# Optimization experiments

Hardware: AMD Instinct MI355X
Metric: run time of the kernel (lower is better)

The kernel has to match this reference:

```python
import jax, jax.numpy as jnp
import numpy as np

EMB = 256
HEADS = 4
HD = EMB // HEADS
BS, SZ = 4, 64


def _layernorm(x, g, b, eps=1e-5):
    mu = jnp.mean(x, axis=-1, keepdims=True)
    var = jnp.mean((x - mu) ** 2, axis=-1, keepdims=True)
    return (x - mu) * jax.lax.rsqrt(var + eps) * g + b


def setup_inputs() -> dict:
    key = jax.random.key(0)
    ks = jax.random.split(key, 12)
    s = lambda k, shape, sc: jax.random.normal(k, shape, jnp.float32) * sc
    return {
        "x": s(ks[0], (BS, EMB, SZ, SZ), 1.0),
        "ln1_g": jnp.ones((EMB,), jnp.float32),
        "ln1_b": jnp.zeros((EMB,), jnp.float32),
        "wq": s(ks[1], (HD, HD), HD ** -0.5), "bq": jnp.zeros((HD,), jnp.float32),
        "wk": s(ks[2], (HD, HD), HD ** -0.5), "bk": jnp.zeros((HD,), jnp.float32),
        "wv": s(ks[3], (HD, HD), HD ** -0.5), "bv": jnp.zeros((HD,), jnp.float32),
        "wo": s(ks[4], (EMB, EMB), EMB ** -0.5), "bo": jnp.zeros((EMB,), jnp.float32),
        "ln2_g": jnp.ones((EMB,), jnp.float32),
        "ln2_b": jnp.zeros((EMB,), jnp.float32),
        "w1": s(ks[5], (EMB, EMB), EMB ** -0.5), "b1": jnp.zeros((EMB,), jnp.float32),
        "w2": s(ks[6], (EMB, EMB), EMB ** -0.5), "b2": jnp.zeros((EMB,), jnp.float32),
    }


def reference(x, ln1_g, ln1_b, wq, bq, wk, bk, wv, bv, wo, bo, ln2_g, ln2_b, w1, b1, w2, b2):
    bs, c, sz, _ = x.shape
    seq = sz * sz
    xt = x.reshape(bs, c, seq).swapaxes(1, 2)  # [b, s, c]
    xn = _layernorm(xt, ln1_g, ln1_b)
    # split heads: [b, h, s, d]
    h = xn.reshape(bs, seq, HEADS, HD).transpose(0, 2, 1, 3)
    q = h @ wq + bq
    k = h @ wk + bk
    v = h @ wv + bv
    scores = jnp.einsum("bhqd,bhkd->bhqk", q, k) / (HD ** 0.5)
    attn = jax.nn.softmax(scores, axis=-1)
    o = jnp.einsum("bhqk,bhkd->bhqd", attn, v)
    o = o.transpose(0, 2, 1, 3).reshape(bs, seq, c)
    o = o @ wo + bo
    av = o + xt  # residual 1
    ff = _layernorm(av, ln2_g, ln2_b) @ w1 + b1
    ff = jax.nn.gelu(ff, approximate=False) @ w2 + b2
    out = ff + av  # residual 2
    return out.swapaxes(1, 2).reshape(bs, c, sz, sz)
```

## Files before the change

### kernel.cpp

```cpp
#include <hip/hip_runtime.h>
#include <hip/hip_bf16.h>
#include <cstdint>

typedef __attribute__((ext_vector_type(8))) short short8;
typedef __attribute__((ext_vector_type(4))) short short4_;
typedef __attribute__((ext_vector_type(4))) float float4_;

#define MFMA16(a,b,c)  __builtin_amdgcn_mfma_f32_16x16x32_bf16(a,b,c,0,0,0)
#define MFMA16K16(a,b,c) __builtin_amdgcn_mfma_f32_16x16x16bf16_1k(a,b,c,0,0,0)
#define EXP2(x) __builtin_amdgcn_exp2f(x)

__device__ __forceinline__ short f2bs(float f) {
    union { float f; uint32_t u; } c;
    c.f = f;
    c.u += 0x7FFF + ((c.u >> 16) & 1);
    return (short)(c.u >> 16);
}
__device__ __forceinline__ float s2f(short s) {
    union { uint32_t u; float f; } c;
    c.u = ((uint32_t)(uint16_t)s) << 16;
    return c.f;
}

static const int EMB = 256;
static const int SEQ = 4096;
static const int TOK = 16384;

#define QSCALE 0.18033688011112042f

__global__ __launch_bounds__(256) void repack_kernel(
    const float* wq, const float* wk, const float* wv,
    const float* wo, const float* w1, const float* w2,
    short* wqT, short* wkT, short* wvT, short* woT, short* w1T, short* w2T)
{
    int idx = blockIdx.x * 256 + threadIdx.x;
    if (idx < 3 * 4096) {
        int m = idx / 4096, r = idx % 4096;
        int n = r / 64, k = r % 64;
        const float* src = (m == 0) ? wq : (m == 1) ? wk : wv;
        short* dst = (m == 0) ? wqT : (m == 1) ? wkT : wvT;
        float v = src[k * 64 + n];
        if (m == 0) v *= QSCALE;
        dst[n * 64 + k] = f2bs(v);
    } else {
        int idx2 = idx - 3 * 4096;
        if (idx2 < 3 * 65536) {
            int m = idx2 / 65536, r = idx2 % 65536;
            int n = r / 256, k = r % 256;
            const float* src = (m == 0) ? wo : (m == 1) ? w1 : w2;
            short* dst = (m == 0) ? woT : (m == 1) ? w1T : w2T;
            dst[n * 256 + k] = f2bs(src[k * 256 + n]);
        }
    }
}

__global__ __launch_bounds__(64) void ln1_kernel(
    const float* x, const float* g, const float* bta,
    short* xn, short* xt)
{
    int t = blockIdx.x * 64 + threadIdx.x;
    int b = t >> 12, sp = t & 4095;
    const float* xb = x + (size_t)b * EMB * SEQ + sp;
    float sum = 0.f, ss = 0.f;
#pragma unroll 32
    for (int c = 0; c < 256; c++) {
        float v = xb[(size_t)c * SEQ];
        sum += v; ss += v * v;
    }
    float mu = sum * (1.f / 256.f);
    float var = ss * (1.f / 256.f) - mu * mu;
    float rs = rsqrtf(var + 1e-5f);
    short* xnr = xn + (size_t)t * 256;
    short* xtr = xt + (size_t)t * 256;
#pragma unroll 8
    for (int c = 0; c < 256; c += 4) {
        short4_ ra, na;
#pragma unroll
        for (int j = 0; j < 4; j++) {
            float v = xb[(size_t)(c + j) * SEQ];
            ra[j] = f2bs(v);
            na[j] = f2bs((v - mu) * rs * g[c + j] + bta[c + j]);
        }
        *(short4_*)(xtr + c) = ra;
        *(short4_*)(xnr + c) = na;
    }
}

__global__ __launch_bounds__(256) void qkv_kernel(
    const short* xn, const short* wqT, const short* wkT, const short* wvT,
    const float* bq, const float* bk, const float* bv,
    short* qo, short* ko, short* vto)
{
    int tid = threadIdx.x;
    int w = tid >> 6, lane = tid & 63, quad = lane >> 4, l15 = lane & 15;
    int m0 = blockIdx.x * 64 + w * 16;
    int row = m0 + l15;
    int bb = row >> 12;
    int s0 = (m0 & 4095) + quad * 4;

    short8 a0[4], a1[4];
#pragma unroll
    for (int h = 0; h < 4; h++) {
        a0[h] = *(const short8*)(xn + (size_t)row * 256 + h * 64 + quad * 8);
        a1[h] = *(const short8*)(xn + (size_t)row * 256 + h * 64 + 32 + quad * 8);
    }

#pragma unroll
    for (int p = 0; p < 3; p++) {
        const short* WT = (p == 0) ? wqT : (p == 1) ? wkT : wvT;
        const float* bias = (p == 0) ? bq : (p == 1) ? bk : bv;
        float bscale = (p == 0) ? QSCALE : 1.f;
#pragma unroll
        for (int nb = 0; nb < 4; nb++) {
            int col = nb * 16 + l15;
            short8 b0 = *(const short8*)(WT + col * 64 + quad * 8);
            short8 b1 = *(const short8*)(WT + col * 64 + 32 + quad * 8);
            float bvv = bias[col] * bscale;
#pragma unroll
            for (int h = 0; h < 4; h++) {
                float4_ acc = {bvv, bvv, bvv, bvv};
                acc = MFMA16(a0[h], b0, acc);
                acc = MFMA16(a1[h], b1, acc);
                size_t headbase = (size_t)(bb * 4 + h) * SEQ;
                if (p < 2) {
                    short* dst = (p == 0) ? qo : ko;
#pragma unroll
                    for (int r = 0; r < 4; r++)
                        dst[(headbase + s0 + r) * 64 + col] = f2bs(acc[r]);
                } else {
                    short4_ pk;
#pragma unroll
                    for (int r = 0; r < 4; r++) pk[r] = f2bs(acc[r]);
                    *(short4_*)(vto + ((size_t)(bb * 4 + h) * 64 + col) * SEQ + s0) = pk;
                }
            }
        }
    }
}

__global__ __attribute__((amdgpu_flat_work_group_size(256, 256),
                          amdgpu_waves_per_eu(4, 4)))
void flash_kernel(
    const short* q, const short* k, const short* vt,
    short* O0, short* O1, float* l0, float* l1)
{
    __shared__ short K_lds[64 * 64];
    __shared__ short V_lds[64 * 64];

    int tid = threadIdx.x;
    int w = tid >> 6, lane = tid & 63, quad = lane >> 4, l15 = lane & 15;
    int qt = blockIdx.x, bh = blockIdx.y, grp = blockIdx.z;
    int span = 64 / gridDim.z;

    const short* qb = q + (size_t)bh * SEQ * 64;
    const short* kb = k + (size_t)bh * SEQ * 64 + (size_t)grp * span * 64 * 64;
    const short* vb = vt + (size_t)bh * 64 * SEQ + grp * span * 64;

    int qrow0 = qt * 128 + w * 32 + l15;
    int qrow1 = qrow0 + 16;
    short8 qA0 = *(const short8*)(qb + (size_t)qrow0 * 64 + quad * 8);
    short8 qA1 = *(const short8*)(qb + (size_t)qrow0 * 64 + 32 + quad * 8);
    short8 qB0 = *(const short8*)(qb + (size_t)qrow1 * 64 + quad * 8);
    short8 qB1 = *(const short8*)(qb + (size_t)qrow1 * 64 + 32 + quad * 8);

    float4_ oacc0[4], oacc1[4];
#pragma unroll
    for (int md = 0; md < 4; md++) {
        oacc0[md] = {0.f, 0.f, 0.f, 0.f};
        oacc1[md] = {0.f, 0.f, 0.f, 0.f};
    }
    float li0 = 0.f, li1 = 0.f;

    int srow = tid >> 2;
    int sr7 = srow & 7;
    int c0 = tid & 3;
    int l7 = l15 & 7;

    int dcA = (c0 ^ sr7) << 3;
    int dcB = ((c0 + 4) ^ sr7) << 3;

    short8 kr0 = *(const short8*)(kb + (size_t)srow * 64 + c0 * 8);
    short8 kr1 = *(const short8*)(kb + (size_t)srow * 64 + (c0 + 4) * 8);
    short8 vr0 = *(const short8*)(vb + (size_t)srow * SEQ + c0 * 8);
    short8 vr1 = *(const short8*)(vb + (size_t)srow * SEQ + (c0 + 4) * 8);

    for (int kt = 0; kt < span; kt++) {
        __syncthreads();
        *(short8*)&K_lds[srow * 64 + dcA] = kr0;
        *(short8*)&K_lds[srow * 64 + dcB] = kr1;
        *(short8*)&V_lds[srow * 64 + dcA] = vr0;
        *(short8*)&V_lds[srow * 64 + dcB] = vr1;
        if (kt + 1 < span) {
            kr0 = *(const short8*)(kb + (size_t)((kt + 1) * 64 + srow) * 64 + c0 * 8);
            kr1 = *(const short8*)(kb + (size_t)((kt + 1) * 64 + srow) * 64 + (c0 + 4) * 8);
            vr0 = *(const short8*)(vb + (size_t)srow * SEQ + (kt + 1) * 64 + c0 * 8);
            vr1 = *(const short8*)(vb + (size_t)srow * SEQ + (kt + 1) * 64 + (c0 + 4) * 8);
        }
        asm volatile("s_waitcnt lgkmcnt(0)" ::: "memory");
        __builtin_amdgcn_s_barrier();
        asm volatile("" ::: "memory");

        short4_ pf0[4], pf1[4];
#pragma unroll
        for (int nb = 0; nb < 4; nb++) {
            short8 k0 = *(const short8*)&K_lds[(nb * 16 + l15) * 64 + ((quad ^ l7) << 3)];
            short8 k1 = *(const short8*)&K_lds[(nb * 16 + l15) * 64 + (((quad + 4) ^ l7) << 3)];
            float4_ a = {0.f, 0.f, 0.f, 0.f};
            a = MFMA16(k0, qA0, a);
            a = MFMA16(k1, qA1, a);
            float4_ b = {0.f, 0.f, 0.f, 0.f};
            b = MFMA16(k0, qB0, b);
            b = MFMA16(k1, qB1, b);

            float p00 = EXP2(a[0]), p01 = EXP2(a[1]);
            float p02 = EXP2(a[2]), p03 = EXP2(a[3]);
            li0 += (p00 + p01) + (p02 + p03);
            float p10 = EXP2(b[0]), p11 = EXP2(b[1]);
            float p12 = EXP2(b[2]), p13 = EXP2(b[3]);
            li1 += (p10 + p11) + (p12 + p13);
            union { short4_ s; uint32_t u[2]; } pa, pb;
            asm("v_cvt_pk_bf16_f32 %0, %1, %2" : "=v"(pa.u[0]) : "v"(p00), "v"(p01));
            asm("v_cvt_pk_bf16_f32 %0, %1, %2" : "=v"(pa.u[1]) : "v"(p02), "v"(p03));
            asm("v_cvt_pk_bf16_f32 %0, %1, %2" : "=v"(pb.u[0]) : "v"(p10), "v"(p11));
            asm("v_cvt_pk_bf16_f32 %0, %1, %2" : "=v"(pb.u[1]) : "v"(p12), "v"(p13));
            pf0[nb] = pa.s;
            pf1[nb] = pb.s;
        }

        __builtin_amdgcn_s_setprio(1);
#pragma unroll
        for (int md = 0; md < 4; md++)
#pragma unroll
            for (int nb = 0; nb < 4; nb++) {
                int c = nb * 2 + (quad >> 1);
                short4_ vf = *(const short4_*)&V_lds[(md * 16 + l15) * 64 +
                                                     ((c ^ l7) << 3) + ((quad & 1) << 2)];
                oacc0[md] = MFMA16K16(vf, pf0[nb], oacc0[md]);
                oacc1[md] = MFMA16K16(vf, pf1[nb], oacc1[md]);
            }
        __builtin_amdgcn_s_setprio(0);
    }

    li0 += __shfl_xor(li0, 16);
    li0 += __shfl_xor(li0, 32);
    li1 += __shfl_xor(li1, 16);
    li1 += __shfl_xor(li1, 32);

    short* Op = grp ? O1 : O0;
    float* lp = grp ? l1 : l0;
    if (quad == 0) {
        lp[bh * 4096 + qrow0] = li0;
        lp[bh * 4096 + qrow1] = li1;
    }

    size_t ob0 = ((size_t)bh * 4096 + qrow0) * 64;
    size_t ob1 = ((size_t)bh * 4096 + qrow1) * 64;
#pragma unroll
    for (int md = 0; md < 4; md++) {
        short4_ pk0, pk1;
#pragma unroll
        for (int r = 0; r < 4; r++) {
            pk0[r] = f2bs(oacc0[md][r]);
            pk1[r] = f2bs(oacc1[md][r]);
        }
        *(short4_*)(Op + ob0 + md * 16 + quad * 4) = pk0;
        *(short4_*)(Op + ob1 + md * 16 + quad * 4) = pk1;
    }
}

__global__ __launch_bounds__(256) void combine_kernel(
    const short* O0, const short* O1, const float* l0, const float* l1,
    short* Oout, int two)
{
    int g = blockIdx.x * 256 + threadIdx.x;
    int qi = g >> 4;
    short4_ a = *(const short4_*)(O0 + (size_t)g * 4);
    float l = l0[qi];
    float4_ acc = {s2f(a[0]), s2f(a[1]), s2f(a[2]), s2f(a[3])};
    if (two) {
        short4_ b = *(const short4_*)(O1 + (size_t)g * 4);
        l += l1[qi];
#pragma unroll
        for (int j = 0; j < 4; j++) acc[j] += s2f(b[j]);
    }
    float inv = 1.f / l;
    short4_ pk;
#pragma unroll
    for (int j = 0; j < 4; j++) pk[j] = f2bs(acc[j] * inv);
    *(short4_*)(Oout + (size_t)g * 4) = pk;
}

__global__ __launch_bounds__(256) void mlp_kernel(
    const short* O0, const short* O1, const float* l0, const float* l1, int two,
    const short* woT, const short* w1T, const short* w2T,
    const float* bo, const float* b1, const float* b2,
    const float* g2, const float* be2,
    const short* xt, float* outf)
{
    __shared__ __align__(16) char smem[3 * 8448 + 128];
    short* av = (short*)smem;
    short* x2 = (short*)(smem + 8448);
    short* ff = (short*)(smem + 16896);
    float* stats = (float*)(smem + 25344);
    float* T = (float*)smem;

    int tid = threadIdx.x;
    int w = tid >> 6, lane = tid & 63, quad = lane >> 4, l15 = lane & 15;
    int m0 = blockIdx.x * 16;
    int n0 = w * 64;
    int arow = m0 + l15;
    int bbA = arow >> 12, spA = arow & 4095;

    float invh[4];
    if (two) {
#pragma unroll
        for (int h = 0; h < 4; h++) {
            size_t li = (size_t)(bbA * 4 + h) * 4096 + spA;
            invh[h] = 1.f / (l0[li] + l1[li]);
        }
    }

    float4_ acc[4];
#pragma unroll
    for (int nb = 0; nb < 4; nb++) {
        float bvv = bo[n0 + nb * 16 + l15];
        acc[nb] = {bvv, bvv, bvv, bvv};
    }
    for (int kc = 0; kc < 8; kc++) {
        int h = kc >> 1;
        int off = (kc & 1) * 32 + quad * 8;
        size_t obase = ((size_t)(bbA * 4 + h) * 4096 + spA) * 64 + off;
        short8 a;
        if (two) {
            short8 a0v = *(const short8*)(O0 + obase);
            short8 a1v = *(const short8*)(O1 + obase);
            float iv = invh[h];
            union { short8 s; uint32_t u[4]; } pa;
#pragma unroll
            for (int jj = 0; jj < 4; jj++) {
                float f0 = (s2f(a0v[2 * jj]) + s2f(a1v[2 * jj])) * iv;
                float f1 = (s2f(a0v[2 * jj + 1]) + s2f(a1v[2 * jj + 1])) * iv;
                asm("v_cvt_pk_bf16_f32 %0, %1, %2" : "=v"(pa.u[jj]) : "v"(f0), "v"(f1));
            }
            a = pa.s;
        } else {
            a = *(const short8*)(O0 + obase);
        }
#pragma unroll
        for (int nb = 0; nb < 4; nb++) {
            short8 b = *(const short8*)(woT + (size_t)(n0 + nb * 16 + l15) * 256 + kc * 32 + quad * 8);
            acc[nb] = MFMA16(a, b, acc[nb]);
        }
    }
#pragma unroll
    for (int nb = 0; nb < 4; nb++) {
        int col = n0 + nb * 16 + l15;
#pragma unroll
        for (int r = 0; r < 4; r++) {
            size_t t = (size_t)m0 + quad * 4 + r;
            av[(quad * 4 + r) * 264 + col] = f2bs(acc[nb][r] + s2f(xt[t * 256 + col]));
        }
    }
    __syncthreads();

    {
        int row = tid >> 4, sub = tid & 15;
        float sum = 0.f, ss = 0.f;
        short8 v0 = *(const short8*)&av[row * 264 + sub * 16];
        short8 v1 = *(const short8*)&av[row * 264 + sub * 16 + 8];
#pragma unroll
        for (int j = 0; j < 8; j++) {
            float a = s2f(v0[j]), b = s2f(v1[j]);
            sum += a + b; ss += a * a + b * b;
        }
#pragma unroll
        for (int off = 1; off < 16; off <<= 1) {
            sum += __shfl_xor(sum, off);
            ss += __shfl_xor(ss, off);
        }
        if (sub == 0) {
            float mu = sum * (1.f / 256.f);
            float var = ss * (1.f / 256.f) - mu * mu;
            stats[row] = mu;
            stats[16 + row] = rsqrtf(var + 1e-5f);
        }
    }
    __syncthreads();

    {
        int row = tid >> 4, sub = tid & 15;
        float mu = stats[row], rs = stats[16 + row];
#pragma unroll
        for (int j = 0; j < 16; j += 4) {
            int c = sub * 16 + j;
            short4_ rv = *(const short4_*)&av[row * 264 + c];
            short4_ pk;
#pragma unroll
            for (int i = 0; i < 4; i++)
                pk[i] = f2bs((s2f(rv[i]) - mu) * rs * g2[c + i] + be2[c + i]);
            *(short4_*)&x2[row * 264 + c] = pk;
        }
    }
    __syncthreads();

#pragma unroll
    for (int nb = 0; nb < 4; nb++) {
        float bvv = b1[n0 + nb * 16 + l15];
        acc[nb] = {bvv, bvv, bvv, bvv};
    }
    for (int kc = 0; kc < 8; kc++) {
        short8 a = *(const short8*)&x2[l15 * 264 + kc * 32 + quad * 8];
#pragma unroll
        for (int nb = 0; nb < 4; nb++) {
            short8 b = *(const short8*)(w1T + (size_t)(n0 + nb * 16 + l15) * 256 + kc * 32 + quad * 8);
            acc[nb] = MFMA16(a, b, acc[nb]);
        }
    }
#pragma unroll
    for (int nb = 0; nb < 4; nb++) {
        int col = n0 + nb * 16 + l15;
#pragma unroll
        for (int r = 0; r < 4; r++) {
            float v = acc[nb][r];
            v = 0.5f * v * (1.f + erff(v * 0.70710678118f));
            ff[(quad * 4 + r) * 264 + col] = f2bs(v);
        }
    }
    __syncthreads();

#pragma unroll
    for (int nb = 0; nb < 4; nb++) {
        float bvv = b2[n0 + nb * 16 + l15];
        acc[nb] = {bvv, bvv, bvv, bvv};
    }
    for (int kc = 0; kc < 8; kc++) {
        short8 a = *(const short8*)&ff[l15 * 264 + kc * 32 + quad * 8];
#pragma unroll
        for (int nb = 0; nb < 4; nb++) {
            short8 b = *(const short8*)(w2T + (size_t)(n0 + nb * 16 + l15) * 256 + kc * 32 + quad * 8);
            acc[nb] = MFMA16(a, b, acc[nb]);
        }
    }
    float vout[4][4];
#pragma unroll
    for (int nb = 0; nb < 4; nb++) {
        int col = n0 + nb * 16 + l15;
#pragma unroll
        for (int r = 0; r < 4; r++)
            vout[nb][r] = acc[nb][r] + s2f(av[(quad * 4 + r) * 264 + col]);
    }
    __syncthreads();

    float* tw = T + w * 1040;
#pragma unroll
    for (int nb = 0; nb < 4; nb++)
#pragma unroll
        for (int r = 0; r < 4; r++)
            tw[(quad * 4 + r) * 65 + nb * 16 + l15] = vout[nb][r];

    int bb = m0 >> 12;
    int spb = m0 & 4095;
    float* dst = outf + ((size_t)bb * 256 + n0 + lane) * SEQ + spb;
#pragma unroll
    for (int j = 0; j < 16; j += 4) {
        float4_ pk = {tw[(j + 0) * 65 + lane], tw[(j + 1) * 65 + lane],
                      tw[(j + 2) * 65 + lane], tw[(j + 3) * 65 + lane]};
        *(float4_*)(dst + j) = pk;
    }
}

extern "C" void kernel_launch(void* const* d_in, const int* in_sizes, int n_in,
                              void* d_out, int out_size, void* d_ws, size_t ws_size,
                              hipStream_t stream)
{
    const float* x     = (const float*)d_in[0];
    const float* ln1_g = (const float*)d_in[1];
    const float* ln1_b = (const float*)d_in[2];
    const float* wq    = (const float*)d_in[3];
    const float* bq    = (const float*)d_in[4];
    const float* wk    = (const float*)d_in[5];
    const float* bk    = (const float*)d_in[6];
    const float* wv    = (const float*)d_in[7];
    const float* bv    = (const float*)d_in[8];
    const float* wo    = (const float*)d_in[9];
    const float* bo    = (const float*)d_in[10];
    const float* ln2_g = (const float*)d_in[11];
    const float* ln2_b = (const float*)d_in[12];
    const float* w1    = (const float*)d_in[13];
    const float* b1    = (const float*)d_in[14];
    const float* w2    = (const float*)d_in[15];
    const float* b2    = (const float*)d_in[16];

    char* ws = (char*)d_ws;
    const size_t SZ_BF = (size_t)TOK * 256 * 2;

    short* wqT = (short*)(ws + 0);
    short* wkT = (short*)(ws + 8192);
    short* wvT = (short*)(ws + 16384);
    short* woT = (short*)(ws + 24576);
    short* w1T = (short*)(ws + 155648);
    short* w2T = (short*)(ws + 286720);
    char* base = ws + 524288;

    short* xt  = (short*)(base);
    short* kbuf= (short*)(base + SZ_BF);
    short* vtb = (short*)(base + 2 * SZ_BF);
    float* l0  = (float*)(base + 3 * SZ_BF);
    float* l1  = (float*)(base + 3 * SZ_BF + 262144);
    short* O1  = (short*)(base + 3 * SZ_BF + 524288);
    short* O0w = (short*)(base + 4 * SZ_BF + 524288);

    const size_t NEED_SPLIT = 524288 + 3 * SZ_BF + 524288 + SZ_BF;
    const size_t NEED_FUSED = 524288 + 5 * SZ_BF + 524288;
    int nz = (ws_size >= NEED_SPLIT) ? 2 : 1;
    int fuse = (nz == 2 && ws_size >= NEED_FUSED);

    short* qb  = (short*)d_out;
    short* xn  = (short*)((char*)d_out + SZ_BF);
    short* O0  = fuse ? O0w : xn;
    short* Onrm= vtb;

    repack_kernel<<<816, 256, 0, stream>>>(wq, wk, wv, wo, w1, w2,
                                           wqT, wkT, wvT, woT, w1T, w2T);
    ln1_kernel<<<TOK / 64, 64, 0, stream>>>(x, ln1_g, ln1_b, xn, xt);
    qkv_kernel<<<TOK / 64, 256, 0, stream>>>(xn, wqT, wkT, wvT, bq, bk, bv,
                                             qb, kbuf, vtb);
    flash_kernel<<<dim3(32, 16, nz), 256, 0, stream>>>(qb, kbuf, vtb, O0, O1, l0, l1);
    if (fuse) {
        mlp_kernel<<<TOK / 16, 256, 0, stream>>>(O0, O1, l0, l1, 2,
                                                 woT, w1T, w2T, bo, b1, b2,
                                                 ln2_g, ln2_b, xt, (float*)d_out);
    } else {
        combine_kernel<<<4096, 256, 0, stream>>>(O0, O1, l0, l1, Onrm, nz - 1);
        mlp_kernel<<<TOK / 16, 256, 0, stream>>>(Onrm, O1, l0, l1, 0,
                                                 woT, w1T, w2T, bo, b1, b2,
                                                 ln2_g, ln2_b, xt, (float*)d_out);
    }
}
```

Measured before the change: 280.3 us.

## Split flash attention KV range four ways and parallelize LN1 over channels

Flash attention can now split the key range into up to four partitions when workspace allows. Partial outputs and row sums are stored in strided buffers and reduced in the combine or fused MLP kernel. The LN1 kernel now spreads each token's 256 channels over 8 thread groups, holds values in registers and reduces through shared memory, so x is read once instead of twice. The flash waves_per_eu bound is also relaxed. The four-way split adds partial-output traffic and reduction work to gain more blocks in flight.

```diff
diff --git a/kernel.cpp b/kernel.cpp
--- a/kernel.cpp
+++ b/kernel.cpp
@@ -25,6 +25,9 @@
 static const int EMB = 256;
 static const int SEQ = 4096;
 static const int TOK = 16384;
+
+static const size_t SZO = 4194304;
+static const size_t LSTRIDE = 65536;
 
 #define QSCALE 0.18033688011112042f
 
@@ -54,35 +57,49 @@
     }
 }
 
-__global__ __launch_bounds__(64) void ln1_kernel(
+__global__ __launch_bounds__(256) void ln1_kernel(
     const float* x, const float* g, const float* bta,
     short* xn, short* xt)
 {
-    int t = blockIdx.x * 64 + threadIdx.x;
+    __shared__ float redS[4][32], redQ[4][32];
+    int tid = threadIdx.x;
+    int l = tid & 31;
+    int p = tid >> 5;
+    int t = blockIdx.x * 32 + l;
     int b = t >> 12, sp = t & 4095;
-    const float* xb = x + (size_t)b * EMB * SEQ + sp;
+    const float* xb = x + (size_t)b * EMB * SEQ + (size_t)(p * 32) * SEQ + sp;
+
+    float v[32];
     float sum = 0.f, ss = 0.f;
-#pragma unroll 32
-    for (int c = 0; c < 256; c++) {
-        float v = xb[(size_t)c * SEQ];
-        sum += v; ss += v * v;
-    }
-    float mu = sum * (1.f / 256.f);
-    float var = ss * (1.f / 256.f) - mu * mu;
+#pragma unroll
+    for (int j = 0; j < 32; j++) {
+        v[j] = xb[(size_t)j * SEQ];
+        sum += v[j]; ss += v[j] * v[j];
+    }
+    sum += __shfl_xor(sum, 32);
+    ss  += __shfl_xor(ss, 32);
+    int w = tid >> 6;
+    if ((tid & 32) == 0) { redS[w][l] = sum; redQ[w][l] = ss; }
+    __syncthreads();
+    float S = (redS[0][l] + redS[1][l]) + (redS[2][l] + redS[3][l]);
+    float Q = (redQ[0][l] + redQ[1][l]) + (redQ[2][l] + redQ[3][l]);
+    float mu = S * (1.f / 256.f);
+    float var = Q * (1.f / 256.f) - mu * mu;
     float rs = rsqrtf(var + 1e-5f);
-    short* xnr = xn + (size_t)t * 256;
-    short* xtr = xt + (size_t)t * 256;
-#pragma unroll 8
-    for (int c = 0; c < 256; c += 4) {
-        short4_ ra, na;
-#pragma unroll
-        for (int j = 0; j < 4; j++) {
-            float v = xb[(size_t)(c + j) * SEQ];
-            ra[j] = f2bs(v);
-            na[j] = f2bs((v - mu) * rs * g[c + j] + bta[c + j]);
-        }
-        *(short4_*)(xtr + c) = ra;
-        *(short4_*)(xnr + c) = na;
+
+    short* xnr = xn + (size_t)t * 256 + p * 32;
+    short* xtr = xt + (size_t)t * 256 + p * 32;
+#pragma unroll
+    for (int c = 0; c < 32; c += 8) {
+        short8 ra, na;
+#pragma unroll
+        for (int j = 0; j < 8; j++) {
+            float vv = v[c + j];
+            ra[j] = f2bs(vv);
+            na[j] = f2bs((vv - mu) * rs * g[p * 32 + c + j] + bta[p * 32 + c + j]);
+        }
+        *(short8*)(xtr + c) = ra;
+        *(short8*)(xnr + c) = na;
     }
 }
 
@@ -139,10 +156,10 @@
 }
 
 __global__ __attribute__((amdgpu_flat_work_group_size(256, 256),
-                          amdgpu_waves_per_eu(4, 4)))
+                          amdgpu_waves_per_eu(4, 8)))
 void flash_kernel(
     const short* q, const short* k, const short* vt,
-    short* O0, short* O1, float* l0, float* l1)
+    short* O0, short* Orest, float* lbase)
 {
     __shared__ short K_lds[64 * 64];
     __shared__ short V_lds[64 * 64];
@@ -246,8 +263,8 @@
     li1 += __shfl_xor(li1, 16);
     li1 += __shfl_xor(li1, 32);
 
-    short* Op = grp ? O1 : O0;
-    float* lp = grp ? l1 : l0;
+    short* Op = grp ? (Orest + (size_t)(grp - 1) * SZO) : O0;
+    float* lp = lbase + (size_t)grp * LSTRIDE;
     if (quad == 0) {
         lp[bh * 4096 + qrow0] = li0;
         lp[bh * 4096 + qrow1] = li1;
@@ -269,19 +286,19 @@
 }
 
 __global__ __launch_bounds__(256) void combine_kernel(
-    const short* O0, const short* O1, const float* l0, const float* l1,
-    short* Oout, int two)
+    const short* O0, const short* Orest, const float* lb,
+    short* Oout, int np)
 {
     int g = blockIdx.x * 256 + threadIdx.x;
     int qi = g >> 4;
     short4_ a = *(const short4_*)(O0 + (size_t)g * 4);
-    float l = l0[qi];
+    float l = lb[qi];
     float4_ acc = {s2f(a[0]), s2f(a[1]), s2f(a[2]), s2f(a[3])};
-    if (two) {
-        short4_ b = *(const short4_*)(O1 + (size_t)g * 4);
-        l += l1[qi];
-#pragma unroll
-        for (int j = 0; j < 4; j++) acc[j] += s2f(b[j]);
+    for (int j = 1; j < np; j++) {
+        short4_ b = *(const short4_*)(Orest + (size_t)(j - 1) * SZO + (size_t)g * 4);
+        l += lb[(size_t)j * LSTRIDE + qi];
+#pragma unroll
+        for (int jj = 0; jj < 4; jj++) acc[jj] += s2f(b[jj]);
     }
     float inv = 1.f / l;
     short4_ pk;
@@ -291,7 +308,7 @@
 }
 
 __global__ __launch_bounds__(256) void mlp_kernel(
-    const short* O0, const short* O1, const float* l0, const float* l1, int two,
+    const short* O0, const short* Orest, const float* lb, int np,
     const short* woT, const short* w1T, const short* w2T,
     const float* bo, const float* b1, const float* b2,
     const float* g2, const float* be2,
@@ -312,11 +329,13 @@
     int bbA = arow >> 12, spA = arow & 4095;
 
     float invh[4];
-    if (two) {
+    if (np) {
 #pragma unroll
         for (int h = 0; h < 4; h++) {
             size_t li = (size_t)(bbA * 4 + h) * 4096 + spA;
-            invh[h] = 1.f / (l0[li] + l1[li]);
+            float s = lb[li];
+            for (int j = 1; j < np; j++) s += lb[(size_t)j * LSTRIDE + li];
+            invh[h] = 1.f / s;
         }
     }
 
@@ -331,15 +350,22 @@
         int off = (kc & 1) * 32 + quad * 8;
         size_t obase = ((size_t)(bbA * 4 + h) * 4096 + spA) * 64 + off;
         short8 a;
-        if (two) {
+        if (np) {
             short8 a0v = *(const short8*)(O0 + obase);
-            short8 a1v = *(const short8*)(O1 + obase);
+            float f[8];
+#pragma unroll
+            for (int jj = 0; jj < 8; jj++) f[jj] = s2f(a0v[jj]);
+            for (int j = 1; j < np; j++) {
+                short8 apv = *(const short8*)(Orest + (size_t)(j - 1) * SZO + obase);
+#pragma unroll
+                for (int jj = 0; jj < 8; jj++) f[jj] += s2f(apv[jj]);
+            }
             float iv = invh[h];
             union { short8 s; uint32_t u[4]; } pa;
 #pragma unroll
             for (int jj = 0; jj < 4; jj++) {
-                float f0 = (s2f(a0v[2 * jj]) + s2f(a1v[2 * jj])) * iv;
-                float f1 = (s2f(a0v[2 * jj + 1]) + s2f(a1v[2 * jj + 1])) * iv;
+                float f0 = f[2 * jj] * iv;
+                float f1 = f[2 * jj + 1] * iv;
                 asm("v_cvt_pk_bf16_f32 %0, %1, %2" : "=v"(pa.u[jj]) : "v"(f0), "v"(f1));
             }
             a = pa.s;
@@ -505,15 +531,29 @@
     short* xt  = (short*)(base);
     short* kbuf= (short*)(base + SZ_BF);
     short* vtb = (short*)(base + 2 * SZ_BF);
-    float* l0  = (float*)(base + 3 * SZ_BF);
-    float* l1  = (float*)(base + 3 * SZ_BF + 262144);
-    short* O1  = (short*)(base + 3 * SZ_BF + 524288);
-    short* O0w = (short*)(base + 4 * SZ_BF + 524288);
-
-    const size_t NEED_SPLIT = 524288 + 3 * SZ_BF + 524288 + SZ_BF;
-    const size_t NEED_FUSED = 524288 + 5 * SZ_BF + 524288;
-    int nz = (ws_size >= NEED_SPLIT) ? 2 : 1;
-    int fuse = (nz == 2 && ws_size >= NEED_FUSED);
+
+    const size_t need2_fb = 524288 + 3 * SZ_BF + 524288 + SZ_BF;
+    const size_t need2_fu = need2_fb + SZ_BF;
+    const size_t need4_fb = 524288 + 3 * SZ_BF + 1048576 + 3 * SZ_BF;
+    const size_t need4_fu = need4_fb + SZ_BF;
+
+    int nz, fuse;
+    if (ws_size >= need4_fb)      { nz = 4; fuse = (ws_size >= need4_fu); }
+    else if (ws_size >= need2_fb) { nz = 2; fuse = (ws_size >= need2_fu); }
+    else                          { nz = 1; fuse = 0; }
+
+    float* lbase;
+    short* Orest;
+    short* O0w;
+    if (nz == 4) {
+        lbase = (float*)(base + 3 * SZ_BF);
+        Orest = (short*)(base + 3 * SZ_BF + 1048576);
+        O0w   = Orest + 3 * SZO;
+    } else {
+        lbase = (float*)(base + 3 * SZ_BF);
+        Orest = (short*)(base + 3 * SZ_BF + 524288);
+        O0w   = Orest + SZO;
+    }
 
     short* qb  = (short*)d_out;
     short* xn  = (short*)((char*)d_out + SZ_BF);
@@ -522,17 +562,17 @@
 
     repack_kernel<<<816, 256, 0, stream>>>(wq, wk, wv, wo, w1, w2,
                                            wqT, wkT, wvT, woT, w1T, w2T);
-    ln1_kernel<<<TOK / 64, 64, 0, stream>>>(x, ln1_g, ln1_b, xn, xt);
+    ln1_kernel<<<TOK / 32, 256, 0, stream>>>(x, ln1_g, ln1_b, xn, xt);
     qkv_kernel<<<TOK / 64, 256, 0, stream>>>(xn, wqT, wkT, wvT, bq, bk, bv,
                                              qb, kbuf, vtb);
-    flash_kernel<<<dim3(32, 16, nz), 256, 0, stream>>>(qb, kbuf, vtb, O0, O1, l0, l1);
+    flash_kernel<<<dim3(32, 16, nz), 256, 0, stream>>>(qb, kbuf, vtb, O0, Orest, lbase);
     if (fuse) {
-        mlp_kernel<<<TOK / 16, 256, 0, stream>>>(O0, O1, l0, l1, 2,
+        mlp_kernel<<<TOK / 16, 256, 0, stream>>>(O0, Orest, lbase, nz,
                                                  woT, w1T, w2T, bo, b1, b2,
                                                  ln2_g, ln2_b, xt, (float*)d_out);
     } else {
-        combine_kernel<<<4096, 256, 0, stream>>>(O0, O1, l0, l1, Onrm, nz - 1);
-        mlp_kernel<<<TOK / 16, 256, 0, stream>>>(Onrm, O1, l0, l1, 0,
+        combine_kernel<<<4096, 256, 0, stream>>>(O0, Orest, lbase, Onrm, nz);
+        mlp_kernel<<<TOK / 16, 256, 0, stream>>>(Onrm, Orest, lbase, 0,
                                                  woT, w1T, w2T, bo, b1, b2,
                                                  ln2_g, ln2_b, xt, (float*)d_out);
     }
```

Result: faster. 271.5 us (-3.1%).
